# Performance work log

Measured on AMD Instinct MI355X. Metric: run time of the kernel, lower is better.

## Reference

```python
import jax, jax.numpy as jnp
import numpy as np

N_USERS = 20000
N_ITEMS = 20000
H0, H1, H2 = 256, 512, 256  # hidden = [256, 512, 256]
B = 4096
LN_EPS = 1e-5


def _ln(x, g, b):
    m = jnp.mean(x, axis=-1, keepdims=True)
    v = jnp.mean(jnp.square(x - m), axis=-1, keepdims=True)
    return (x - m) * jax.lax.rsqrt(v + LN_EPS) * g + b


def setup_inputs() -> dict:
    key = jax.random.key(0)
    ks = jax.random.split(key, 12)
    s = 0.02
    inp = {
        "user_idx": jax.random.randint(ks[0], (B,), 0, N_USERS),
        "item_idx": jax.random.randint(ks[1], (B,), 0, N_ITEMS),
        # (n_users+1, n_items+1) binary interaction matrix, stored as bool
        "interactions": jax.random.bernoulli(ks[2], 0.05, (N_USERS + 1, N_ITEMS + 1)),
        # proj_u / proj_i (bias=False), torch Linear layout (out, in)
        "Wu": jax.random.normal(ks[3], (H0, N_ITEMS), jnp.float32) * s,
        "Wi": jax.random.normal(ks[4], (H0, N_USERS), jnp.float32) * s,
        # rep_u: Linear(H0,H1)+LN+ReLU, Linear(H1,H2)+LN+ReLU (dropout=eval identity)
        "W1": jax.random.normal(ks[5], (H1, H0), jnp.float32) * s,
        "b1": jnp.zeros((H1,), jnp.float32),
        "g1": jnp.ones((H1,), jnp.float32),
        "be1": jnp.zeros((H1,), jnp.float32),
        "W2": jax.random.normal(ks[6], (H2, H1), jnp.float32) * s,
        "b2": jnp.zeros((H2,), jnp.float32),
        "g2": jnp.ones((H2,), jnp.float32),
        "be2": jnp.zeros((H2,), jnp.float32),
        # logit layer
        "Wl": jax.random.normal(ks[7], (1, H2), jnp.float32) * s,
        "bl": jnp.zeros((1,), jnp.float32),
    }
    return inp


def reference(user_idx, item_idx, interactions, Wu, Wi, W1, b1, g1, be1,
              W2, b2, g2, be2, Wl, bl):
    b_arange = jnp.arange(user_idx.shape[0])

    # --- user history embedding: gather row, zero target item, project, MLP ---
    u_slice = interactions[user_idx, :-1].astype(jnp.float32)      # (B, n_items)
    u_slice = u_slice.at[b_arange, item_idx].set(0.0)
    u = u_slice @ Wu.T                                             # (B, H0)
    u = jax.nn.relu(_ln(u @ W1.T + b1, g1, be1))                   # (B, H1)
    user_rep = jax.nn.relu(_ln(u @ W2.T + b2, g2, be2))            # (B, H2)

    # --- item history embedding: gather column, zero target user, project ---
    i_slice = interactions.T[item_idx][:, :-1].astype(jnp.float32)  # (B, n_users)
    i_slice = i_slice.at[b_arange, user_idx].set(0.0)
    item_rep = i_slice @ Wi.T                                      # (B, H0); rep_i is an empty Sequential in source

    pred_vector = user_rep * item_rep                              # (B, H2) == (B, H0)
    logit = (pred_vector @ Wl.T + bl).squeeze(-1)                  # (B,)
    return logit
```

## Files before the change

### kernel.cpp

```cpp
#include <hip/hip_runtime.h>

#define N_USERS 20000
#define N_ITEMS 20000
#define NI1     20001
#define HB      4096
#define H0      256
#define H1      512
#define H2      256
#define PKW     632
#define PKB     (PKW*4)
#define NWF     12501251

typedef unsigned short u16;
typedef unsigned char  u8;
typedef unsigned int   u32;
typedef unsigned long long u64;

typedef __attribute__((ext_vector_type(8))) __bf16 bf16x8;
typedef __attribute__((ext_vector_type(4))) float  f32x4;

__device__ __forceinline__ u16 f2bf(float f) {
  u32 u = __float_as_uint(f);
  u32 r = (u + 0x7FFFu + ((u >> 16) & 1u)) >> 16;
  return (u16)r;
}

__global__ __launch_bounds__(256) void k_detect(const u8* __restrict__ inter,
                                                int* __restrict__ flag) {
  __shared__ u32 cnt[4];
  if (threadIdx.x < 4) cnt[threadIdx.x] = 0;
  __syncthreads();
  u32 loc0 = 0, loc1 = 0, loc2 = 0, loc3 = 0;
  for (int i = threadIdx.x; i < 16384; i += 256) {
    u32 w = ((const u32*)inter)[i];
    loc0 += (w & 0x000000FFu) ? 1u : 0u;
    loc1 += (w & 0x0000FF00u) ? 1u : 0u;
    loc2 += (w & 0x00FF0000u) ? 1u : 0u;
    loc3 += (w & 0xFF000000u) ? 1u : 0u;
  }
  atomicAdd(&cnt[0], loc0); atomicAdd(&cnt[1], loc1);
  atomicAdd(&cnt[2], loc2); atomicAdd(&cnt[3], loc3);
  __syncthreads();
  if (threadIdx.x == 0) {
    int lay;
    if (cnt[1] != 0)      lay = 0;
    else if (cnt[0] != 0) lay = 1;
    else                  lay = 2;
    *flag = lay;
  }
}

__global__ __launch_bounds__(256) void k_packF(const u8* __restrict__ inter,
                                               u32* __restrict__ pkF,
                                               const int* __restrict__ flag) {
  int lay = *flag;
  __shared__ u32 nibs[4][8][64];
  const size_t TE = (size_t)NI1 * NI1;
  const int NG = (int)((TE + 8191) / 8192);
  int wave = threadIdx.x >> 6, lane = threadIdx.x & 63;
  const u32* base32 = (const u32*)inter;
  for (int g = blockIdx.x; g < NG; g += gridDim.x) {
    size_t E0 = (size_t)g * 8192 + (size_t)wave * 2048;
    bool full = ((size_t)(g + 1) * 8192) <= TE;
    if (lay != 0) {
      if (full) {
        #pragma unroll
        for (int t = 0; t < 8; ++t) {
          size_t e = E0 + (size_t)t * 256 + lane * 4;
          uint4 v = *(const uint4*)(base32 + e);
          nibs[wave][t][lane] = (v.x ? 1u : 0u) | (v.y ? 2u : 0u) |
                                (v.z ? 4u : 0u) | (v.w ? 8u : 0u);
        }
      } else {
        #pragma unroll
        for (int t = 0; t < 8; ++t) {
          size_t e = E0 + (size_t)t * 256 + lane * 4;
          u32 n = 0;
          #pragma unroll
          for (int c = 0; c < 4; ++c)
            if (e + c < TE && base32[e + c]) n |= 1u << c;
          nibs[wave][t][lane] = n;
        }
      }
    } else {
      #pragma unroll
      for (int t = 0; t < 8; ++t) {
        size_t e = E0 + (size_t)t * 256 + lane * 4;
        u32 n = 0;
        #pragma unroll
        for (int c = 0; c < 4; ++c)
          if (e + c < TE && inter[e + c]) n |= 1u << c;
        nibs[wave][t][lane] = n;
      }
    }
    __syncthreads();
    {
      int t = lane >> 3, j = lane & 7;
      u32 wrd = 0;
      #pragma unroll
      for (int k = 0; k < 8; ++k) wrd |= nibs[wave][t][8 * j + k] << (4 * k);
      size_t wg = (size_t)g * 256 + wave * 64 + lane;
      if (wg < NWF) pkF[wg] = wrd;
    }
    __syncthreads();
  }
}

__global__ __launch_bounds__(256) void k_realign(const u32* __restrict__ pkF,
                                                 u32* __restrict__ pk) {
  int r = blockIdx.x;
  int base = 625 * r + (r >> 5);
  int s = r & 31;
  for (int w = threadIdx.x; w < PKW; w += 256) {
    u32 val = 0;
    if (w < 625) {
      u32 lo = pkF[base + w];
      u32 hi = pkF[base + w + 1];
      val = s ? ((lo >> s) | (hi << (32 - s))) : lo;
    }
    pk[(size_t)r * PKW + w] = val;
  }
}

#define HDSTEP(J, M)                                      \
  _Pragma("unroll")                                       \
  for (int k = 0; k < 32; ++k) if (!(k & J)) {            \
    u32 tt = (a[k] ^ (a[k | J] >> J)) & M;                \
    a[k] ^= tt; a[k | J] ^= tt << J;                      \
  }

__global__ __launch_bounds__(256) void k_bitT(const u32* __restrict__ pk,
                                              u32* __restrict__ pkT) {
  __shared__ u32 in_l[512][17];
  __shared__ u32 out_l[32][16][17];
  int t = threadIdx.x;
  int vt = blockIdx.x % 40, wt = blockIdx.x / 40;
  int v0 = vt * 16, wc0 = wt * 16;
  int lw = t & 15, lr = t >> 4;
  for (int ch = 0; ch < 32; ++ch) {
    int rloc = ch * 16 + lr;
    int R = v0 * 32 + rloc;
    int W = wc0 + lw;
    u32 val = 0;
    if (R < N_USERS && W < PKW) val = pk[(size_t)R * PKW + W];
    in_l[rloc][lw] = val;
  }
  __syncthreads();
  u32 a[32];
  #pragma unroll
  for (int j = 0; j < 32; ++j) a[j] = in_l[lr * 32 + j][lw];
  HDSTEP(16, 0x0000FFFFu)
  HDSTEP(8,  0x00FF00FFu)
  HDSTEP(4,  0x0F0F0F0Fu)
  HDSTEP(2,  0x33333333u)
  HDSTEP(1,  0x55555555u)
  #pragma unroll
  for (int i = 0; i < 32; ++i) out_l[i][lw][lr] = __brev(a[31 - i]);
  __syncthreads();
  for (int ch = 0; ch < 32; ++ch) {
    int rloc = ch * 16 + lr;
    int C = wc0 * 32 + rloc;
    int V = v0 + lw;
    if (C < N_ITEMS && V < PKW)
      pkT[(size_t)C * PKW + V] = out_l[rloc & 31][rloc >> 5][lw];
  }
}

__global__ __launch_bounds__(256) void k_convert2(const float* __restrict__ Wu,
                                                  const float* __restrict__ Wi,
                                                  u16* __restrict__ Wub,
                                                  u16* __restrict__ Wib) {
  const int n4 = H0 * N_ITEMS / 4;
  int stride = gridDim.x * 256;
  for (int i = blockIdx.x * 256 + threadIdx.x; i < 2 * n4; i += stride) {
    const float* in = (i < n4) ? Wu : Wi;
    u16* out = (i < n4) ? Wub : Wib;
    int idx = (i < n4) ? i : i - n4;
    float4 v = ((const float4*)in)[idx];
    u64 p = (u64)f2bf(v.x) | ((u64)f2bf(v.y) << 16) |
            ((u64)f2bf(v.z) << 32) | ((u64)f2bf(v.w) << 48);
    ((u64*)out)[idx] = p;
  }
}

__global__ __launch_bounds__(256) void k_transpose2(const float* __restrict__ W1,
                                                    float* __restrict__ W1T,
                                                    const float* __restrict__ W2,
                                                    float* __restrict__ W2T) {
  __shared__ float tile[32][33];
  int bid = blockIdx.x;
  const float* in; float* out; int R, C, b;
  if (bid < 128) { in = W1; out = W1T; R = H1; C = H0; b = bid; }
  else           { in = W2; out = W2T; R = H2; C = H1; b = bid - 128; }
  int nbx = C >> 5;
  int bx = b % nbx, by = b / nbx;
  int c0 = bx * 32, r0 = by * 32;
  int lx = threadIdx.x & 31, ly = threadIdx.x >> 5;
  #pragma unroll
  for (int j = 0; j < 4; ++j)
    tile[ly + 8*j][lx] = in[(size_t)(r0 + ly + 8*j) * C + c0 + lx];
  __syncthreads();
  #pragma unroll
  for (int j = 0; j < 4; ++j)
    out[(size_t)(c0 + ly + 8*j) * R + r0 + lx] = tile[lx][ly + 8*j];
}

__global__ __launch_bounds__(1024) void k_sort(const int* __restrict__ item_idx,
                                               int* __restrict__ perm) {
  __shared__ u32 cnt[N_ITEMS];
  __shared__ u32 tsum[1024];
  int t = threadIdx.x;
  for (int i = t; i < N_ITEMS; i += 1024) cnt[i] = 0;
  __syncthreads();
  for (int b = t; b < HB; b += 1024) atomicAdd(&cnt[item_idx[b]], 1u);
  __syncthreads();
  u32 s = 0;
  int base = t * 20;
  for (int j = 0; j < 20; ++j) { int i = base + j; if (i < N_ITEMS) s += cnt[i]; }
  tsum[t] = s;
  __syncthreads();
  for (int off = 1; off < 1024; off <<= 1) {
    u32 v = (t >= off) ? tsum[t - off] : 0u;
    __syncthreads();
    tsum[t] += v;
    __syncthreads();
  }
  u32 run = tsum[t] - s;
  for (int j = 0; j < 20; ++j) {
    int i = base + j;
    if (i < N_ITEMS) { u32 c = cnt[i]; cnt[i] = run; run += c; }
  }
  __syncthreads();
  for (int b = t; b < HB; b += 1024) {
    int v = item_idx[b];
    u32 pos = atomicAdd(&cnt[v], 1u);
    perm[pos] = b;
  }
}

__global__ __launch_bounds__(256) void k_gemm(
    const u32* __restrict__ pk, const u32* __restrict__ pkT,
    const int* __restrict__ user_idx, const int* __restrict__ item_idx,
    const int* __restrict__ perm,
    const u16* __restrict__ Wub, const u16* __restrict__ Wib,
    float* __restrict__ u0, float* __restrict__ ir) {
  __shared__ __attribute__((aligned(16))) u16 Bls[32 * 128];
  __shared__ __attribute__((aligned(16))) uint2 lut8[16];
  __shared__ u32 pbase[128];
  __shared__ int prow[128];

  int bid = blockIdx.x;
  int mode_item = bid >> 8;
  int lid = bid & 255;
  int M0 = (lid >> 3) * 128;
  int N0 = (lid & 7) * 32;
  int tid = threadIdx.x;
  const u16* Wb = mode_item ? Wib : Wub;
  const u8* Pk = (const u8*)(mode_item ? pkT : pk);
  float* Cout = mode_item ? ir : u0;

  if (tid < 16) {
    u32 v = tid;
    lut8[tid].x = ((v & 1u) ? 0x3F80u : 0u) | ((v & 2u) ? 0x3F800000u : 0u);
    lut8[tid].y = ((v & 4u) ? 0x3F80u : 0u) | ((v & 8u) ? 0x3F800000u : 0u);
  }
  if (tid < 128) {
    int s = M0 + tid;
    if (mode_item) { int p = perm[s]; prow[tid] = p; pbase[tid] = (u32)item_idx[p] * PKB; }
    else           { prow[tid] = s;   pbase[tid] = (u32)user_idx[s] * PKB; }
  }
  __syncthreads();

  f32x4 acc[2][2];
  #pragma unroll
  for (int a = 0; a < 2; ++a)
    #pragma unroll
    for (int b = 0; b < 2; ++b)
      #pragma unroll
      for (int j = 0; j < 4; ++j) acc[a][b][j] = 0.f;

  int lane = tid & 63, wave = tid >> 6;
  int WM = wave * 32;
  int lrow = lane & 15;
  int lk8 = lane >> 4;
  int sh = lk8 * 8;

  u32 pb0 = pbase[WM + lrow];
  u32 pb1 = pbase[WM + 16 + lrow];

  for (int k0 = 0; k0 < 20096; k0 += 128) {
    #pragma unroll
    for (int i = 0; i < 2; ++i) {
      int id = tid + 256 * i;
      int n = id >> 4, c8 = id & 15;
      int k = k0 + c8 * 8;
      uint4 v = make_uint4(0u, 0u, 0u, 0u);
      if (k < N_ITEMS) v = *(const uint4*)&Wb[(size_t)(N0 + n) * N_ITEMS + k];
      int off = n * 128 + ((c8 * 8) ^ ((n & 7) << 3));
      *(uint4*)&Bls[off] = v;
    }
    uint4 qa0 = *(const uint4*)(Pk + pb0 + (k0 >> 3));
    uint4 qa1 = *(const uint4*)(Pk + pb1 + (k0 >> 3));
    u32 qw0[4] = {qa0.x, qa0.y, qa0.z, qa0.w};
    u32 qw1[4] = {qa1.x, qa1.y, qa1.z, qa1.w};
    __syncthreads();
    #pragma unroll
    for (int kki = 0; kki < 4; ++kki) {
      u32 b0 = (qw0[kki] >> sh) & 0xFFu;
      u32 b1 = (qw1[kki] >> sh) & 0xFFu;
      union { u32 w[4]; bf16x8 v; } a0, a1;
      uint2 l0 = lut8[b0 & 15u], h0 = lut8[b0 >> 4];
      uint2 l1 = lut8[b1 & 15u], h1 = lut8[b1 >> 4];
      a0.w[0] = l0.x; a0.w[1] = l0.y; a0.w[2] = h0.x; a0.w[3] = h0.y;
      a1.w[0] = l1.x; a1.w[1] = l1.y; a1.w[2] = h1.x; a1.w[3] = h1.y;
      bf16x8 bfr[2];
      #pragma unroll
      for (int fn = 0; fn < 2; ++fn) {
        int n = fn * 16 + lrow;
        bfr[fn] = *(const bf16x8*)&Bls[n * 128 + ((kki * 32 + sh) ^ ((n & 7) << 3))];
      }
      acc[0][0] = __builtin_amdgcn_mfma_f32_16x16x32_bf16(a0.v, bfr[0], acc[0][0], 0, 0, 0);
      acc[0][1] = __builtin_amdgcn_mfma_f32_16x16x32_bf16(a0.v, bfr[1], acc[0][1], 0, 0, 0);
      acc[1][0] = __builtin_amdgcn_mfma_f32_16x16x32_bf16(a1.v, bfr[0], acc[1][0], 0, 0, 0);
      acc[1][1] = __builtin_amdgcn_mfma_f32_16x16x32_bf16(a1.v, bfr[1], acc[1][1], 0, 0, 0);
    }
    __syncthreads();
  }

  int crow0 = (lane >> 4) * 4;
  int ccol = lane & 15;
  #pragma unroll
  for (int fm = 0; fm < 2; ++fm)
    #pragma unroll
    for (int fn = 0; fn < 2; ++fn) {
      f32x4 v = acc[fm][fn];
      int col = N0 + fn * 16 + ccol;
      #pragma unroll
      for (int j = 0; j < 4; ++j) {
        int rl = WM + fm * 16 + crow0 + j;
        Cout[(size_t)prow[rl] * H0 + col] = v[j];
      }
    }
}

__global__ __launch_bounds__(256) void k_mlp(
    const u32* __restrict__ pk,
    const int* __restrict__ user_idx, const int* __restrict__ item_idx,
    const float* __restrict__ Wu, const float* __restrict__ Wi,
    const float* __restrict__ u0, const float* __restrict__ ir,
    const float* __restrict__ W1T, const float* __restrict__ b1,
    const float* __restrict__ g1, const float* __restrict__ be1,
    const float* __restrict__ W2T, const float* __restrict__ b2,
    const float* __restrict__ g2, const float* __restrict__ be2,
    const float* __restrict__ Wl, const float* __restrict__ bl,
    float* __restrict__ out) {
  __shared__ __attribute__((aligned(16))) float xl[16][H0];
  __shared__ __attribute__((aligned(16))) float h1l[16][H1];
  __shared__ int flagL[16], uL[16], iL[16];

  int tid = threadIdx.x, lane = tid & 63, wave = tid >> 6;
  int b0 = blockIdx.x * 16;

  if (tid < 16) {
    int b = b0 + tid;
    int uu = user_idx[b], ii = item_idx[b];
    uL[tid] = uu; iL[tid] = ii;
    u8 byte = ((const u8*)pk)[(size_t)uu * PKB + (ii >> 3)];
    flagL[tid] = (byte >> (ii & 7)) & 1;
  }
  __syncthreads();

  for (int idx = tid; idx < 16 * H0; idx += 256) {
    int rr = idx >> 8, h = idx & 255;
    float x = u0[(size_t)(b0 + rr) * H0 + h];
    if (flagL[rr]) x -= Wu[(size_t)h * N_ITEMS + iL[rr]];
    xl[rr][h] = x;
  }
  __syncthreads();

  float a0[16], a1[16];
  #pragma unroll
  for (int rr = 0; rr < 16; ++rr) { a0[rr] = 0.f; a1[rr] = 0.f; }
  for (int k4 = 0; k4 < H0 / 4; ++k4) {
    int k = k4 * 4;
    float w0a = W1T[(size_t)(k+0)*H1 + tid], w0b = W1T[(size_t)(k+0)*H1 + tid + 256];
    float w1a = W1T[(size_t)(k+1)*H1 + tid], w1b = W1T[(size_t)(k+1)*H1 + tid + 256];
    float w2a = W1T[(size_t)(k+2)*H1 + tid], w2b = W1T[(size_t)(k+2)*H1 + tid + 256];
    float w3a = W1T[(size_t)(k+3)*H1 + tid], w3b = W1T[(size_t)(k+3)*H1 + tid + 256];
    #pragma unroll
    for (int rr = 0; rr < 16; ++rr) {
      float4 x = *(const float4*)&xl[rr][k];
      a0[rr] += x.x * w0a + x.y * w1a + x.z * w2a + x.w * w3a;
      a1[rr] += x.x * w0b + x.y * w1b + x.z * w2b + x.w * w3b;
    }
  }
  #pragma unroll
  for (int rr = 0; rr < 16; ++rr) {
    h1l[rr][tid]       = a0[rr] + b1[tid];
    h1l[rr][tid + 256] = a1[rr] + b1[tid + 256];
  }
  __syncthreads();

  for (int rr = wave; rr < 16; rr += 4) {
    float s = 0.f;
    #pragma unroll
    for (int j = 0; j < 8; ++j) s += h1l[rr][lane + 64 * j];
    #pragma unroll
    for (int off = 32; off; off >>= 1) s += __shfl_xor(s, off);
    float m = s * (1.f / H1);
    float v = 0.f;
    #pragma unroll
    for (int j = 0; j < 8; ++j) { float d = h1l[rr][lane + 64*j] - m; v += d * d; }
    #pragma unroll
    for (int off = 32; off; off >>= 1) v += __shfl_xor(v, off);
    float inv = rsqrtf(v * (1.f / H1) + 1e-5f);
    #pragma unroll
    for (int j = 0; j < 8; ++j) {
      int o = lane + 64 * j;
      float y = (h1l[rr][o] - m) * inv * g1[o] + be1[o];
      h1l[rr][o] = fmaxf(y, 0.f);
    }
  }
  __syncthreads();

  float a2[16];
  #pragma unroll
  for (int rr = 0; rr < 16; ++rr) a2[rr] = 0.f;
  for (int k4 = 0; k4 < H1 / 4; ++k4) {
    int k = k4 * 4;
    float w0 = W2T[(size_t)(k+0)*H2 + tid];
    float w1 = W2T[(size_t)(k+1)*H2 + tid];
    float w2 = W2T[(size_t)(k+2)*H2 + tid];
    float w3 = W2T[(size_t)(k+3)*H2 + tid];
    #pragma unroll
    for (int rr = 0; rr < 16; ++rr) {
      float4 x = *(const float4*)&h1l[rr][k];
      a2[rr] += x.x * w0 + x.y * w1 + x.z * w2 + x.w * w3;
    }
  }
  __syncthreads();
  #pragma unroll
  for (int rr = 0; rr < 16; ++rr) xl[rr][tid] = a2[rr] + b2[tid];
  __syncthreads();

  for (int rr = wave; rr < 16; rr += 4) {
    float s = 0.f;
    #pragma unroll
    for (int j = 0; j < 4; ++j) s += xl[rr][lane + 64 * j];
    #pragma unroll
    for (int off = 32; off; off >>= 1) s += __shfl_xor(s, off);
    float m = s * (1.f / H2);
    float v = 0.f;
    #pragma unroll
    for (int j = 0; j < 4; ++j) { float d = xl[rr][lane + 64*j] - m; v += d * d; }
    #pragma unroll
    for (int off = 32; off; off >>= 1) v += __shfl_xor(v, off);
    float inv = rsqrtf(v * (1.f / H2) + 1e-5f);
    #pragma unroll
    for (int j = 0; j < 4; ++j) {
      int o = lane + 64 * j;
      float y = (xl[rr][o] - m) * inv * g2[o] + be2[o];
      xl[rr][o] = fmaxf(y, 0.f);
    }
  }
  __syncthreads();

  for (int rr = wave; rr < 16; rr += 4) {
    int b = b0 + rr;
    int flg = flagL[rr], uu = uL[rr];
    float s = 0.f;
    #pragma unroll
    for (int j = 0; j < 4; ++j) {
      int h = lane + 64 * j;
      float irv = ir[(size_t)b * H0 + h];
      if (flg) irv -= Wi[(size_t)h * N_USERS + uu];
      s += xl[rr][h] * irv * Wl[h];
    }
    #pragma unroll
    for (int off = 32; off; off >>= 1) s += __shfl_xor(s, off);
    if (lane == 0) out[b] = s + bl[0];
  }
}

extern "C" void kernel_launch(void* const* d_in, const int* in_sizes, int n_in,
                              void* d_out, int out_size, void* d_ws, size_t ws_size,
                              hipStream_t stream) {
  const int*   user_idx = (const int*)d_in[0];
  const int*   item_idx = (const int*)d_in[1];
  const u8*    inter    = (const u8*)d_in[2];
  const float* Wu  = (const float*)d_in[3];
  const float* Wi  = (const float*)d_in[4];
  const float* W1  = (const float*)d_in[5];
  const float* b1  = (const float*)d_in[6];
  const float* g1  = (const float*)d_in[7];
  const float* be1 = (const float*)d_in[8];
  const float* W2  = (const float*)d_in[9];
  const float* b2  = (const float*)d_in[10];
  const float* g2  = (const float*)d_in[11];
  const float* be2 = (const float*)d_in[12];
  const float* Wl  = (const float*)d_in[13];
  const float* bl  = (const float*)d_in[14];
  float* out = (float*)d_out;

  char* ws = (char*)d_ws;
  size_t off = 0;
  auto alloc = [&](size_t bytes) {
    size_t o = off;
    off = (off + bytes + 255) & ~(size_t)255;
    return o;
  };
  int*   flag = (int*)  (ws + alloc(4));
  u32*   pkF  = (u32*)  (ws + alloc((size_t)(NWF + 64) * 4));
  u32*   pk   = (u32*)  (ws + alloc((size_t)N_USERS * PKB));
  u32*   pkT  = (u32*)  (ws + alloc((size_t)N_ITEMS * PKB));
  u16*   Wub  = (u16*)  (ws + alloc((size_t)H0 * N_ITEMS * 2));
  u16*   Wib  = (u16*)  (ws + alloc((size_t)H0 * N_USERS * 2));
  float* W1T  = (float*)(ws + alloc((size_t)H0 * H1 * 4));
  float* W2T  = (float*)(ws + alloc((size_t)H1 * H2 * 4));
  float* u0   = (float*)(ws + alloc((size_t)HB * H0 * 4));
  float* ir   = (float*)(ws + alloc((size_t)HB * H0 * 4));
  int*   perm = (int*)  (ws + alloc((size_t)HB * 4));

  k_detect<<<1, 256, 0, stream>>>(inter, flag);
  k_packF<<<3072, 256, 0, stream>>>(inter, pkF, flag);
  k_realign<<<N_USERS, 256, 0, stream>>>(pkF, pk);
  k_bitT<<<1600, 256, 0, stream>>>(pk, pkT);
  k_convert2<<<1024, 256, 0, stream>>>(Wu, Wi, Wub, Wib);
  k_transpose2<<<256, 256, 0, stream>>>(W1, W1T, W2, W2T);
  k_sort<<<1, 1024, 0, stream>>>(item_idx, perm);
  k_gemm<<<512, 256, 0, stream>>>(pk, pkT, user_idx, item_idx, perm, Wub, Wib, u0, ir);
  k_mlp<<<256, 256, 0, stream>>>(pk, user_idx, item_idx, Wu, Wi, u0, ir,
                                 W1T, b1, g1, be1, W2T, b2, g2, be2, Wl, bl, out);
}
```

Baseline: 719.1 us.

## Split GEMM K dimension in two halves and widen K tile to 256

The bit-packed GEMM is split along K into two halves, doubling the grid to 1024 blocks. Each half writes its own partial output buffer, and the MLP kernel adds the two partials when it loads them. The K tile per iteration grows from 128 to 256, which halves the number of barriers, and launch bounds request 4 waves per EU. The aim is better occupancy and parallelism on a GPU with many CUs, at the cost of extra partial buffers and more write and read traffic.

```diff
diff --git a/kernel.cpp b/kernel.cpp
--- a/kernel.cpp
+++ b/kernel.cpp
@@ -238,26 +238,28 @@
   }
 }
 
-__global__ __launch_bounds__(256) void k_gemm(
+__global__ __launch_bounds__(256, 4) void k_gemm(
     const u32* __restrict__ pk, const u32* __restrict__ pkT,
     const int* __restrict__ user_idx, const int* __restrict__ item_idx,
     const int* __restrict__ perm,
     const u16* __restrict__ Wub, const u16* __restrict__ Wib,
-    float* __restrict__ u0, float* __restrict__ ir) {
-  __shared__ __attribute__((aligned(16))) u16 Bls[32 * 128];
+    float* __restrict__ u0, float* __restrict__ u0b,
+    float* __restrict__ ir, float* __restrict__ irb) {
+  __shared__ __attribute__((aligned(16))) u16 Bls[32 * 256];
   __shared__ __attribute__((aligned(16))) uint2 lut8[16];
   __shared__ u32 pbase[128];
   __shared__ int prow[128];
 
   int bid = blockIdx.x;
-  int mode_item = bid >> 8;
+  int kh = bid >> 9;
+  int mode_item = (bid >> 8) & 1;
   int lid = bid & 255;
   int M0 = (lid >> 3) * 128;
   int N0 = (lid & 7) * 32;
   int tid = threadIdx.x;
   const u16* Wb = mode_item ? Wib : Wub;
   const u8* Pk = (const u8*)(mode_item ? pkT : pk);
-  float* Cout = mode_item ? ir : u0;
+  float* Cout = mode_item ? (kh ? irb : ir) : (kh ? u0b : u0);
 
   if (tid < 16) {
     u32 v = tid;
@@ -288,24 +290,30 @@
   u32 pb0 = pbase[WM + lrow];
   u32 pb1 = pbase[WM + 16 + lrow];
 
-  for (int k0 = 0; k0 < 20096; k0 += 128) {
-    #pragma unroll
-    for (int i = 0; i < 2; ++i) {
+  int k0_beg = kh ? 10240 : 0;
+  int k0_end = kh ? 20224 : 10240;
+
+  for (int k0 = k0_beg; k0 < k0_end; k0 += 256) {
+    #pragma unroll
+    for (int i = 0; i < 4; ++i) {
       int id = tid + 256 * i;
-      int n = id >> 4, c8 = id & 15;
+      int n = id >> 5, c8 = id & 31;
       int k = k0 + c8 * 8;
       uint4 v = make_uint4(0u, 0u, 0u, 0u);
       if (k < N_ITEMS) v = *(const uint4*)&Wb[(size_t)(N0 + n) * N_ITEMS + k];
-      int off = n * 128 + ((c8 * 8) ^ ((n & 7) << 3));
+      int off = n * 256 + ((c8 * 8) ^ ((n & 7) << 3));
       *(uint4*)&Bls[off] = v;
     }
-    uint4 qa0 = *(const uint4*)(Pk + pb0 + (k0 >> 3));
-    uint4 qa1 = *(const uint4*)(Pk + pb1 + (k0 >> 3));
-    u32 qw0[4] = {qa0.x, qa0.y, qa0.z, qa0.w};
-    u32 qw1[4] = {qa1.x, qa1.y, qa1.z, qa1.w};
+    int bc = k0 >> 3;
+    uint4 qa0l = *(const uint4*)(Pk + pb0 + bc);
+    uint4 qa0h = *(const uint4*)(Pk + pb0 + bc + 16);
+    uint4 qa1l = *(const uint4*)(Pk + pb1 + bc);
+    uint4 qa1h = *(const uint4*)(Pk + pb1 + bc + 16);
+    u32 qw0[8] = {qa0l.x, qa0l.y, qa0l.z, qa0l.w, qa0h.x, qa0h.y, qa0h.z, qa0h.w};
+    u32 qw1[8] = {qa1l.x, qa1l.y, qa1l.z, qa1l.w, qa1h.x, qa1h.y, qa1h.z, qa1h.w};
     __syncthreads();
     #pragma unroll
-    for (int kki = 0; kki < 4; ++kki) {
+    for (int kki = 0; kki < 8; ++kki) {
       u32 b0 = (qw0[kki] >> sh) & 0xFFu;
       u32 b1 = (qw1[kki] >> sh) & 0xFFu;
       union { u32 w[4]; bf16x8 v; } a0, a1;
@@ -317,7 +325,7 @@
       #pragma unroll
       for (int fn = 0; fn < 2; ++fn) {
         int n = fn * 16 + lrow;
-        bfr[fn] = *(const bf16x8*)&Bls[n * 128 + ((kki * 32 + sh) ^ ((n & 7) << 3))];
+        bfr[fn] = *(const bf16x8*)&Bls[n * 256 + ((kki * 32 + sh) ^ ((n & 7) << 3))];
       }
       acc[0][0] = __builtin_amdgcn_mfma_f32_16x16x32_bf16(a0.v, bfr[0], acc[0][0], 0, 0, 0);
       acc[0][1] = __builtin_amdgcn_mfma_f32_16x16x32_bf16(a0.v, bfr[1], acc[0][1], 0, 0, 0);
@@ -347,7 +355,8 @@
     const u32* __restrict__ pk,
     const int* __restrict__ user_idx, const int* __restrict__ item_idx,
     const float* __restrict__ Wu, const float* __restrict__ Wi,
-    const float* __restrict__ u0, const float* __restrict__ ir,
+    const float* __restrict__ u0, const float* __restrict__ u0b,
+    const float* __restrict__ ir, const float* __restrict__ irb,
     const float* __restrict__ W1T, const float* __restrict__ b1,
     const float* __restrict__ g1, const float* __restrict__ be1,
     const float* __restrict__ W2T, const float* __restrict__ b2,
@@ -372,7 +381,8 @@
 
   for (int idx = tid; idx < 16 * H0; idx += 256) {
     int rr = idx >> 8, h = idx & 255;
-    float x = u0[(size_t)(b0 + rr) * H0 + h];
+    size_t o = (size_t)(b0 + rr) * H0 + h;
+    float x = u0[o] + u0b[o];
     if (flagL[rr]) x -= Wu[(size_t)h * N_ITEMS + iL[rr]];
     xl[rr][h] = x;
   }
@@ -472,7 +482,8 @@
     #pragma unroll
     for (int j = 0; j < 4; ++j) {
       int h = lane + 64 * j;
-      float irv = ir[(size_t)b * H0 + h];
+      size_t o = (size_t)b * H0 + h;
+      float irv = ir[o] + irb[o];
       if (flg) irv -= Wi[(size_t)h * N_USERS + uu];
       s += xl[rr][h] * irv * Wl[h];
     }
@@ -518,7 +529,9 @@
   float* W1T  = (float*)(ws + alloc((size_t)H0 * H1 * 4));
   float* W2T  = (float*)(ws + alloc((size_t)H1 * H2 * 4));
   float* u0   = (float*)(ws + alloc((size_t)HB * H0 * 4));
+  float* u0b  = (float*)(ws + alloc((size_t)HB * H0 * 4));
   float* ir   = (float*)(ws + alloc((size_t)HB * H0 * 4));
+  float* irb  = (float*)(ws + alloc((size_t)HB * H0 * 4));
   int*   perm = (int*)  (ws + alloc((size_t)HB * 4));
 
   k_detect<<<1, 256, 0, stream>>>(inter, flag);
@@ -528,7 +541,8 @@
   k_convert2<<<1024, 256, 0, stream>>>(Wu, Wi, Wub, Wib);
   k_transpose2<<<256, 256, 0, stream>>>(W1, W1T, W2, W2T);
   k_sort<<<1, 1024, 0, stream>>>(item_idx, perm);
-  k_gemm<<<512, 256, 0, stream>>>(pk, pkT, user_idx, item_idx, perm, Wub, Wib, u0, ir);
-  k_mlp<<<256, 256, 0, stream>>>(pk, user_idx, item_idx, Wu, Wi, u0, ir,
+  k_gemm<<<1024, 256, 0, stream>>>(pk, pkT, user_idx, item_idx, perm, Wub, Wib,
+                                   u0, u0b, ir, irb);
+  k_mlp<<<256, 256, 0, stream>>>(pk, user_idx, item_idx, Wu, Wi, u0, u0b, ir, irb,
                                  W1T, b1, g1, be1, W2T, b2, g2, be2, Wl, bl, out);
 }
```

Result: faster. 658.8 us (-8.4%).
